# Kernel tuning notes

Hardware: AMD Instinct MI355X
Metric: run time of the kernel (lower is better)

Reference implementation:

```python
import jax, jax.numpy as jnp
import numpy as np

N = 50000      # nodes
E = 500000     # edges
D_IN = 512
D_H = 512
D_OUT = 256


def setup_inputs() -> dict:
    key = jax.random.key(0)
    ks = jax.random.split(key, 5)
    x = jax.random.normal(ks[0], (N, D_IN), dtype=jnp.float32)
    edge_index = jax.random.randint(ks[1], (2, E), 0, N, dtype=jnp.int32)
    W1 = jax.random.normal(ks[2], (D_IN, D_H), dtype=jnp.float32) / np.float32(np.sqrt(D_IN))
    b1 = jnp.zeros((D_H,), dtype=jnp.float32)
    W2 = jax.random.normal(ks[3], (D_H, D_OUT), dtype=jnp.float32) / np.float32(np.sqrt(D_H))
    b2 = jnp.zeros((D_OUT,), dtype=jnp.float32)
    return {"x": x, "edge_index": edge_index, "W1": W1, "b1": b1, "W2": W2, "b2": b2}


def _gcn_conv(x, src, dst, W, b, n):
    # PyG GCNConv: h = X W; add self-loops; symmetric norm D^-1/2 (A+I) D^-1/2; aggregate at dst; + bias
    h = x @ W
    loop = jnp.arange(n, dtype=src.dtype)
    src_sl = jnp.concatenate([src, loop])
    dst_sl = jnp.concatenate([dst, loop])
    deg = jax.ops.segment_sum(jnp.ones_like(src_sl, dtype=h.dtype), dst_sl, num_segments=n)
    dinv = jnp.where(deg > 0, jax.lax.rsqrt(deg), 0.0)
    norm = dinv[src_sl] * dinv[dst_sl]                     # [E+N]
    msg = h[src_sl] * norm[:, None]                        # [E+N, out]
    out = jax.ops.segment_sum(msg, dst_sl, num_segments=n) # [N, out]
    return out + b


def reference(x, edge_index, W1, b1, W2, b2):
    # Encoder.forward in eval mode (dropout = identity, bn='none' = identity), ELU activation after each conv.
    src, dst = edge_index[0], edge_index[1]
    h = _gcn_conv(x, src, dst, W1, b1, N)
    h = jax.nn.elu(h)
    h = _gcn_conv(h, src, dst, W2, b2, N)
    return jax.nn.elu(h)
```

## Files before the change

### kernel.cpp

```cpp
#include <hip/hip_runtime.h>
#include <math.h>

#define N_NODES 50000
#define N_EDGES 500000
#define D_IN 512
#define D_H  512
#define D_OUT 256
#define NB 196

typedef __attribute__((ext_vector_type(8))) short bf16x8;
typedef __attribute__((ext_vector_type(8))) unsigned short ushort8;
typedef __attribute__((ext_vector_type(4))) float f32x4;

__device__ __forceinline__ float b2f(unsigned short u) {
    union { unsigned int i; float f; } v; v.i = ((unsigned int)u) << 16; return v.f;
}
__device__ __forceinline__ unsigned short f2b(float f) {
    unsigned int x = __float_as_uint(f);
    unsigned int r = (x + 0x7fffu + ((x >> 16) & 1u)) >> 16;
    return (unsigned short)r;
}


__global__ __launch_bounds__(256) void k_cvt(const float* __restrict__ in,
                                             unsigned short* __restrict__ out,
                                             long long n8) {
    long long i = (long long)blockIdx.x * 256 + threadIdx.x;
    if (i >= n8) return;
    float4 v0 = ((const float4*)in)[i * 2];
    float4 v1 = ((const float4*)in)[i * 2 + 1];
    ushort8 o;
    o[0] = f2b(v0.x); o[1] = f2b(v0.y); o[2] = f2b(v0.z); o[3] = f2b(v0.w);
    o[4] = f2b(v1.x); o[5] = f2b(v1.y); o[6] = f2b(v1.z); o[7] = f2b(v1.w);
    ((ushort8*)out)[i] = o;
}


__global__ void k_wt(const float* __restrict__ W, unsigned short* __restrict__ Wt,
                     int K, int N) {
    __shared__ float t[32][33];
    const int bk = blockIdx.x * 32, bn = blockIdx.y * 32;
    const int tx = threadIdx.x, ty = threadIdx.y;
    for (int i = ty; i < 32; i += 8) t[i][tx] = W[(size_t)(bk + i) * N + bn + tx];
    __syncthreads();
    for (int i = ty; i < 32; i += 8)
        Wt[(size_t)(bn + i) * K + bk + tx] = f2b(t[tx][i]);
}


__global__ __launch_bounds__(256) void k_zero(int* __restrict__ p, int n) {
    int i = blockIdx.x * 256 + threadIdx.x;
    if (i < n) p[i] = 0;
}

__global__ __launch_bounds__(256) void k_indeg(const int* __restrict__ dst,
                                               int* __restrict__ indeg) {
    int i = blockIdx.x * 256 + threadIdx.x;
    if (i < N_EDGES) atomicAdd(&indeg[dst[i]], 1);
}

__global__ __launch_bounds__(256) void k_partials(const int* __restrict__ indeg,
                                                  int* __restrict__ bsum) {
    __shared__ int wsum[4];
    const int tid = threadIdx.x, lane = tid & 63, w = tid >> 6;
    const int i = blockIdx.x * 256 + tid;
    int v = (i < N_NODES) ? indeg[i] : 0;
#pragma unroll
    for (int o = 32; o > 0; o >>= 1) v += __shfl_down(v, o, 64);
    if (lane == 0) wsum[w] = v;
    __syncthreads();
    if (tid == 0) bsum[blockIdx.x] = wsum[0] + wsum[1] + wsum[2] + wsum[3];
}

__global__ __launch_bounds__(256) void k_scanb(const int* __restrict__ bsum,
                                               int* __restrict__ boff) {
    __shared__ int wsum[4];
    const int tid = threadIdx.x, lane = tid & 63, w = tid >> 6;
    const int v = (tid < NB) ? bsum[tid] : 0;
    int s = v;
#pragma unroll
    for (int o = 1; o < 64; o <<= 1) {
        int t = __shfl_up(s, o, 64);
        if (lane >= o) s += t;
    }
    if (lane == 63) wsum[w] = s;
    __syncthreads();
    int add = 0;
    for (int k = 0; k < w; ++k) add += wsum[k];
    if (tid < NB) boff[tid] = add + s - v;
}

__global__ __launch_bounds__(256) void k_finalize(const int* __restrict__ indeg,
                                                  const int* __restrict__ boff,
                                                  int* __restrict__ row_start,
                                                  int* __restrict__ cursor,
                                                  float* __restrict__ dinv) {
    __shared__ int wsum[4];
    const int tid = threadIdx.x, lane = tid & 63, w = tid >> 6;
    const int i = blockIdx.x * 256 + tid;
    const int v = (i < N_NODES) ? indeg[i] : 0;
    int s = v;
#pragma unroll
    for (int o = 1; o < 64; o <<= 1) {
        int t = __shfl_up(s, o, 64);
        if (lane >= o) s += t;
    }
    if (lane == 63) wsum[w] = s;
    __syncthreads();
    int add = boff[blockIdx.x];
    for (int k = 0; k < w; ++k) add += wsum[k];
    if (i < N_NODES) {
        const int excl = add + s - v;
        row_start[i] = excl;
        cursor[i] = excl;
        dinv[i] = rsqrtf((float)(1 + v));
    }
    if (i == N_NODES) row_start[N_NODES] = N_EDGES;
}

__global__ __launch_bounds__(256) void k_bucket(const int* __restrict__ src,
                                                const int* __restrict__ dst,
                                                int* __restrict__ cursor,
                                                int* __restrict__ csr_src) {
    int e = blockIdx.x * 256 + threadIdx.x;
    if (e >= N_EDGES) return;
    int pos = atomicAdd(&cursor[dst[e]], 1);
    csr_src[pos] = src[e];
}


__device__ __forceinline__ void gload16(const void* g, void* l) {
    __builtin_amdgcn_global_load_lds(
        (const __attribute__((address_space(1))) unsigned int*)g,
        (__attribute__((address_space(3))) unsigned int*)l, 16, 0, 0);
}

__global__ __launch_bounds__(256, 2) void k_gemm(const unsigned short* __restrict__ A,
                                                 const unsigned short* __restrict__ Bt,
                                                 unsigned short* __restrict__ C,
                                                 int M, int N, int K,
                                                 int ncb, int nrb) {
    __shared__ __align__(16) short As[2][128 * 64];
    __shared__ __align__(16) short Bs[2][128 * 64];

    const int bid = blockIdx.x;
    const int xcd = bid & 7;
    const int sidx = bid >> 3;
    const int cb = sidx % ncb;
    const int rb = (sidx / ncb) * 8 + xcd;
    if (rb >= nrb) return;
    const int brow = rb * 128;
    const int bcol = cb * 128;

    const int tid = threadIdx.x;
    const int wid = tid >> 6;
    const int lane = tid & 63;
    const int wr = wid >> 1, wc = wid & 1;
    const int lhi = lane >> 4, llo = lane & 15;

    f32x4 acc[4][4];
#pragma unroll
    for (int i = 0; i < 4; ++i)
#pragma unroll
        for (int j = 0; j < 4; ++j) acc[i][j] = (f32x4){0.f, 0.f, 0.f, 0.f};

#define STAGE(buf, kt)                                                          \
    {                                                                           \
        _Pragma("unroll") for (int g = 0; g < 4; ++g) {                         \
            const int s = g * 256 + tid;                                        \
            const int row = s >> 3;                                             \
            const int sc = (s & 7) ^ (row & 7);                                 \
            int gr = brow + row; gr = gr < M ? gr : M - 1;                      \
            gload16(A + (size_t)gr * K + (kt) + sc * 8,                         \
                    &As[buf][(g * 256 + wid * 64) * 8]);                        \
            gload16(Bt + (size_t)(bcol + row) * K + (kt) + sc * 8,              \
                    &Bs[buf][(g * 256 + wid * 64) * 8]);                        \
        }                                                                       \
    }

    const int nt = K / 64;

    STAGE(0, 0);
    __syncthreads();

    int cur = 0;
    for (int t = 0; t < nt; ++t) {
        if (t + 1 < nt) STAGE(cur ^ 1, (t + 1) * 64);

#pragma unroll
        for (int ks = 0; ks < 2; ++ks) {
            bf16x8 af[4], bf[4];
#pragma unroll
            for (int mi = 0; mi < 4; ++mi) {
                const int row = wr * 64 + mi * 16 + llo;
                af[mi] = *(const bf16x8*)&As[cur][row * 64 + (((ks * 4 + lhi) ^ (llo & 7)) * 8)];
            }
#pragma unroll
            for (int ni = 0; ni < 4; ++ni) {
                const int row = wc * 64 + ni * 16 + llo;
                bf[ni] = *(const bf16x8*)&Bs[cur][row * 64 + (((ks * 4 + lhi) ^ (llo & 7)) * 8)];
            }
#pragma unroll
            for (int mi = 0; mi < 4; ++mi)
#pragma unroll
                for (int ni = 0; ni < 4; ++ni)
                    acc[mi][ni] = __builtin_amdgcn_mfma_f32_16x16x32_bf16(
                        af[mi], bf[ni], acc[mi][ni], 0, 0, 0);
        }

        __syncthreads();
        cur ^= 1;
    }
#undef STAGE

    short* cws = &As[0][0] + wid * 4096;

#pragma unroll
    for (int mi = 0; mi < 4; ++mi)
#pragma unroll
        for (int ni = 0; ni < 4; ++ni) {
            const f32x4 v = acc[mi][ni];
#pragma unroll
            for (int r = 0; r < 4; ++r) {
                const int row = mi * 16 + lhi * 4 + r;
                const int col = ni * 16 + llo;
                const int chunk = (col >> 3) ^ (row & 7);
                cws[row * 64 + chunk * 8 + (col & 7)] = (short)f2b(v[r]);
            }
        }
    __syncthreads();

    {
        const int rsub = lane >> 3;
        const int c = lane & 7;
#pragma unroll
        for (int i = 0; i < 8; ++i) {
            const int row = i * 8 + rsub;
            const ushort8 o = *(const ushort8*)&cws[row * 64 + ((c ^ (row & 7)) * 8)];
            const int grow = brow + wr * 64 + row;
            if (grow < M)
                *(ushort8*)(C + (size_t)grow * N + bcol + wc * 64 + c * 8) = o;
        }
    }
}


template <int D, bool BF16_OUT>
__global__ __launch_bounds__(256) void k_aggregate(const unsigned short* __restrict__ H,
                                                   const float* __restrict__ bias,
                                                   void* __restrict__ outv,
                                                   const int* __restrict__ row_start,
                                                   const int* __restrict__ csr_src,
                                                   const float* __restrict__ dinv) {
    const int wid = threadIdx.x >> 6;
    const int lane = threadIdx.x & 63;
    int n, c0;
    if (D == 512) { n = blockIdx.x * 4 + wid; c0 = lane * 8; }
    else          { n = blockIdx.x * 8 + wid * 2 + (lane >> 5); c0 = (lane & 31) * 8; }
    if (n >= N_NODES) return;

    const float di = dinv[n];
    float acc[8];
    {
        const float ws = di * di;
        ushort8 v = *(const ushort8*)(H + (size_t)n * D + c0);
#pragma unroll
        for (int e = 0; e < 8; ++e) acc[e] = b2f(v[e]) * ws;
    }

    const int e0 = row_start[n];
    const int e1 = row_start[n + 1];
    int j = e0;
    for (; j + 8 <= e1; j += 8) {
        int s[8];
        float wgt[8];
#pragma unroll
        for (int q = 0; q < 8; ++q) s[q] = csr_src[j + q];
#pragma unroll
        for (int q = 0; q < 8; ++q) wgt[q] = dinv[s[q]] * di;
#pragma unroll
        for (int h = 0; h < 2; ++h) {
            const ushort8 v0 = *(const ushort8*)(H + (size_t)s[h * 4 + 0] * D + c0);
            const ushort8 v1 = *(const ushort8*)(H + (size_t)s[h * 4 + 1] * D + c0);
            const ushort8 v2 = *(const ushort8*)(H + (size_t)s[h * 4 + 2] * D + c0);
            const ushort8 v3 = *(const ushort8*)(H + (size_t)s[h * 4 + 3] * D + c0);
#pragma unroll
            for (int e = 0; e < 8; ++e) {
                acc[e] = fmaf(b2f(v0[e]), wgt[h * 4 + 0], acc[e]);
                acc[e] = fmaf(b2f(v1[e]), wgt[h * 4 + 1], acc[e]);
                acc[e] = fmaf(b2f(v2[e]), wgt[h * 4 + 2], acc[e]);
                acc[e] = fmaf(b2f(v3[e]), wgt[h * 4 + 3], acc[e]);
            }
        }
    }
    for (; j + 4 <= e1; j += 4) {
        const int s0 = csr_src[j + 0];
        const int s1 = csr_src[j + 1];
        const int s2 = csr_src[j + 2];
        const int s3 = csr_src[j + 3];
        const float w0 = dinv[s0] * di;
        const float w1 = dinv[s1] * di;
        const float w2 = dinv[s2] * di;
        const float w3 = dinv[s3] * di;
        const ushort8 v0 = *(const ushort8*)(H + (size_t)s0 * D + c0);
        const ushort8 v1 = *(const ushort8*)(H + (size_t)s1 * D + c0);
        const ushort8 v2 = *(const ushort8*)(H + (size_t)s2 * D + c0);
        const ushort8 v3 = *(const ushort8*)(H + (size_t)s3 * D + c0);
#pragma unroll
        for (int e = 0; e < 8; ++e) {
            acc[e] = fmaf(b2f(v0[e]), w0, acc[e]);
            acc[e] = fmaf(b2f(v1[e]), w1, acc[e]);
            acc[e] = fmaf(b2f(v2[e]), w2, acc[e]);
            acc[e] = fmaf(b2f(v3[e]), w3, acc[e]);
        }
    }
    for (; j < e1; ++j) {
        const int s = csr_src[j];
        const float ws = dinv[s] * di;
        const ushort8 v = *(const ushort8*)(H + (size_t)s * D + c0);
#pragma unroll
        for (int e = 0; e < 8; ++e) acc[e] = fmaf(b2f(v[e]), ws, acc[e]);
    }

#pragma unroll
    for (int e = 0; e < 8; ++e) {
        float t = acc[e] + bias[c0 + e];
        acc[e] = t > 0.f ? t : expf(t) - 1.f;
    }

    if (BF16_OUT) {
        ushort8 o;
#pragma unroll
        for (int e = 0; e < 8; ++e) o[e] = f2b(acc[e]);
        *(ushort8*)((unsigned short*)outv + (size_t)n * D + c0) = o;
    } else {
        float* orow = (float*)outv + (size_t)n * D + c0;
        *(float4*)orow = make_float4(acc[0], acc[1], acc[2], acc[3]);
        *(float4*)(orow + 4) = make_float4(acc[4], acc[5], acc[6], acc[7]);
    }
}


extern "C" void kernel_launch(void* const* d_in, const int* in_sizes, int n_in,
                              void* d_out, int out_size, void* d_ws, size_t ws_size,
                              hipStream_t stream) {
    const float* x  = (const float*)d_in[0];
    const int* ei   = (const int*)d_in[1];
    const int* src  = ei;
    const int* dst  = ei + N_EDGES;
    const float* W1 = (const float*)d_in[2];
    const float* b1 = (const float*)d_in[3];
    const float* W2 = (const float*)d_in[4];
    const float* b2 = (const float*)d_in[5];
    float* out = (float*)d_out;

    char* ws = (char*)d_ws;
    size_t off = 0;
    auto alloc = [&](size_t bytes) -> void* {
        void* p = ws + off;
        off = (off + bytes + 255) & ~(size_t)255;
        return p;
    };
    int*   indeg     = (int*)alloc((size_t)N_NODES * 4);
    int*   bsum      = (int*)alloc((size_t)NB * 4);
    int*   boff      = (int*)alloc((size_t)NB * 4);
    int*   row_start = (int*)alloc((size_t)(N_NODES + 1) * 4);
    int*   cursor    = (int*)alloc((size_t)N_NODES * 4);
    int*   csr_src   = (int*)alloc((size_t)N_EDGES * 4);
    float* dinv      = (float*)alloc((size_t)N_NODES * 4);
    unsigned short* W1t  = (unsigned short*)alloc((size_t)D_H * D_IN * 2);
    unsigned short* W2t  = (unsigned short*)alloc((size_t)D_OUT * D_H * 2);
    unsigned short* xb   = (unsigned short*)alloc((size_t)N_NODES * D_IN * 2);
    unsigned short* H1   = (unsigned short*)alloc((size_t)N_NODES * D_H * 2);
    unsigned short* out1 = (unsigned short*)alloc((size_t)N_NODES * D_H * 2);
    unsigned short* H2   = (unsigned short*)alloc((size_t)N_NODES * D_OUT * 2);

    k_zero<<<(N_NODES + 255) / 256, 256, 0, stream>>>(indeg, N_NODES);
    k_indeg<<<(N_EDGES + 255) / 256, 256, 0, stream>>>(dst, indeg);
    k_partials<<<NB, 256, 0, stream>>>(indeg, bsum);
    k_scanb<<<1, 256, 0, stream>>>(bsum, boff);
    k_finalize<<<NB, 256, 0, stream>>>(indeg, boff, row_start, cursor, dinv);
    k_bucket<<<(N_EDGES + 255) / 256, 256, 0, stream>>>(src, dst, cursor, csr_src);

    {
        const long long n8 = (long long)N_NODES * D_IN / 8;
        k_cvt<<<(int)((n8 + 255) / 256), 256, 0, stream>>>(x, xb, n8);
        dim3 b(32, 8);
        dim3 g1(D_IN / 32, D_H / 32);
        k_wt<<<g1, b, 0, stream>>>(W1, W1t, D_IN, D_H);
        dim3 g2(D_H / 32, D_OUT / 32);
        k_wt<<<g2, b, 0, stream>>>(W2, W2t, D_H, D_OUT);
    }

    const int nrb = (N_NODES + 127) / 128;
    const int rgrp = (nrb + 7) / 8;

    {
        const int ncb = D_H / 128;
        k_gemm<<<8 * ncb * rgrp, 256, 0, stream>>>(xb, W1t, H1, N_NODES, D_H, D_IN, ncb, nrb);
    }
    k_aggregate<512, true><<<(N_NODES + 3) / 4, 256, 0, stream>>>(H1, b1, out1, row_start, csr_src, dinv);

    {
        const int ncb = D_OUT / 128;
        k_gemm<<<8 * ncb * rgrp, 256, 0, stream>>>(out1, W2t, H2, N_NODES, D_OUT, D_H, ncb, nrb);
    }
    k_aggregate<256, false><<<(N_NODES + 7) / 8, 256, 0, stream>>>(H2, b2, out, row_start, csr_src, dinv);
}
```

Baseline: 294.8 us.

## Split aggregation into XCD-pinned column chunks for per-XCD L2 reuse

The aggregation kernel is rewritten so that each block covers a 32-column slice for 32 nodes. Block IDs are mapped so that blockIdx mod 8 picks the column chunk, which places each column slice on one XCD and lets its L2 cache hold only that slice of H during the gather. Each lane now loads 8-byte ushort4 values instead of 16-byte vectors, and the 8-edge unrolled loop is dropped. The cost is that csr_src, row_start and dinv are read more times (once per chunk), and the smaller loads plus less unrolling give less memory-level parallelism per thread.

```diff
diff --git a/kernel.cpp b/kernel.cpp
--- a/kernel.cpp
+++ b/kernel.cpp
@@ -245,54 +245,42 @@
 }
 
 
-template <int D, bool BF16_OUT>
-__global__ __launch_bounds__(256) void k_aggregate(const unsigned short* __restrict__ H,
+template <int D, bool BF16_OUT, int NPASS>
+__global__ __launch_bounds__(256) void k_agg_chunk(const unsigned short* __restrict__ H,
                                                    const float* __restrict__ bias,
                                                    void* __restrict__ outv,
                                                    const int* __restrict__ row_start,
                                                    const int* __restrict__ csr_src,
-                                                   const float* __restrict__ dinv) {
-    const int wid = threadIdx.x >> 6;
-    const int lane = threadIdx.x & 63;
-    int n, c0;
-    if (D == 512) { n = blockIdx.x * 4 + wid; c0 = lane * 8; }
-    else          { n = blockIdx.x * 8 + wid * 2 + (lane >> 5); c0 = (lane & 31) * 8; }
+                                                   const float* __restrict__ dinv,
+                                                   int nbpc) {
+    const int bid = blockIdx.x;
+    const int xcd = bid & 7;
+    const int s = bid >> 3;
+    const int pass = s / nbpc;
+    const int nb = s % nbpc;
+    const int col0 = (pass * 8 + xcd) * 32;
+
+    const int tid = threadIdx.x;
+    const int wid = tid >> 6;
+    const int lane = tid & 63;
+    const int grp = lane >> 3;
+    const int lg = lane & 7;
+
+    const int n = nb * 32 + wid * 8 + grp;
     if (n >= N_NODES) return;
+    const int c = col0 + lg * 4;
 
     const float di = dinv[n];
-    float acc[8];
-    {
-        const float ws = di * di;
-        ushort8 v = *(const ushort8*)(H + (size_t)n * D + c0);
-#pragma unroll
-        for (int e = 0; e < 8; ++e) acc[e] = b2f(v[e]) * ws;
+    float a0, a1, a2, a3;
+    {
+        const float w = di * di;
+        ushort4 v = *(const ushort4*)(H + (size_t)n * D + c);
+        a0 = b2f(v.x) * w; a1 = b2f(v.y) * w; a2 = b2f(v.z) * w; a3 = b2f(v.w) * w;
     }
 
     const int e0 = row_start[n];
     const int e1 = row_start[n + 1];
     int j = e0;
-    for (; j + 8 <= e1; j += 8) {
-        int s[8];
-        float wgt[8];
-#pragma unroll
-        for (int q = 0; q < 8; ++q) s[q] = csr_src[j + q];
-#pragma unroll
-        for (int q = 0; q < 8; ++q) wgt[q] = dinv[s[q]] * di;
-#pragma unroll
-        for (int h = 0; h < 2; ++h) {
-            const ushort8 v0 = *(const ushort8*)(H + (size_t)s[h * 4 + 0] * D + c0);
-            const ushort8 v1 = *(const ushort8*)(H + (size_t)s[h * 4 + 1] * D + c0);
-            const ushort8 v2 = *(const ushort8*)(H + (size_t)s[h * 4 + 2] * D + c0);
-            const ushort8 v3 = *(const ushort8*)(H + (size_t)s[h * 4 + 3] * D + c0);
-#pragma unroll
-            for (int e = 0; e < 8; ++e) {
-                acc[e] = fmaf(b2f(v0[e]), wgt[h * 4 + 0], acc[e]);
-                acc[e] = fmaf(b2f(v1[e]), wgt[h * 4 + 1], acc[e]);
-                acc[e] = fmaf(b2f(v2[e]), wgt[h * 4 + 2], acc[e]);
-                acc[e] = fmaf(b2f(v3[e]), wgt[h * 4 + 3], acc[e]);
-            }
-        }
-    }
     for (; j + 4 <= e1; j += 4) {
         const int s0 = csr_src[j + 0];
         const int s1 = csr_src[j + 1];
@@ -302,41 +290,40 @@
         const float w1 = dinv[s1] * di;
         const float w2 = dinv[s2] * di;
         const float w3 = dinv[s3] * di;
-        const ushort8 v0 = *(const ushort8*)(H + (size_t)s0 * D + c0);
-        const ushort8 v1 = *(const ushort8*)(H + (size_t)s1 * D + c0);
-        const ushort8 v2 = *(const ushort8*)(H + (size_t)s2 * D + c0);
-        const ushort8 v3 = *(const ushort8*)(H + (size_t)s3 * D + c0);
-#pragma unroll
-        for (int e = 0; e < 8; ++e) {
-            acc[e] = fmaf(b2f(v0[e]), w0, acc[e]);
-            acc[e] = fmaf(b2f(v1[e]), w1, acc[e]);
-            acc[e] = fmaf(b2f(v2[e]), w2, acc[e]);
-            acc[e] = fmaf(b2f(v3[e]), w3, acc[e]);
-        }
+        const ushort4 v0 = *(const ushort4*)(H + (size_t)s0 * D + c);
+        const ushort4 v1 = *(const ushort4*)(H + (size_t)s1 * D + c);
+        const ushort4 v2 = *(const ushort4*)(H + (size_t)s2 * D + c);
+        const ushort4 v3 = *(const ushort4*)(H + (size_t)s3 * D + c);
+        a0 = fmaf(b2f(v0.x), w0, a0); a1 = fmaf(b2f(v0.y), w0, a1);
+        a2 = fmaf(b2f(v0.z), w0, a2); a3 = fmaf(b2f(v0.w), w0, a3);
+        a0 = fmaf(b2f(v1.x), w1, a0); a1 = fmaf(b2f(v1.y), w1, a1);
+        a2 = fmaf(b2f(v1.z), w1, a2); a3 = fmaf(b2f(v1.w), w1, a3);
+        a0 = fmaf(b2f(v2.x), w2, a0); a1 = fmaf(b2f(v2.y), w2, a1);
+        a2 = fmaf(b2f(v2.z), w2, a2); a3 = fmaf(b2f(v2.w), w2, a3);
+        a0 = fmaf(b2f(v3.x), w3, a0); a1 = fmaf(b2f(v3.y), w3, a1);
+        a2 = fmaf(b2f(v3.z), w3, a2); a3 = fmaf(b2f(v3.w), w3, a3);
     }
     for (; j < e1; ++j) {
-        const int s = csr_src[j];
-        const float ws = dinv[s] * di;
-        const ushort8 v = *(const ushort8*)(H + (size_t)s * D + c0);
-#pragma unroll
-        for (int e = 0; e < 8; ++e) acc[e] = fmaf(b2f(v[e]), ws, acc[e]);
-    }
-
-#pragma unroll
-    for (int e = 0; e < 8; ++e) {
-        float t = acc[e] + bias[c0 + e];
-        acc[e] = t > 0.f ? t : expf(t) - 1.f;
-    }
+        const int sx = csr_src[j];
+        const float w = dinv[sx] * di;
+        const ushort4 v = *(const ushort4*)(H + (size_t)sx * D + c);
+        a0 = fmaf(b2f(v.x), w, a0); a1 = fmaf(b2f(v.y), w, a1);
+        a2 = fmaf(b2f(v.z), w, a2); a3 = fmaf(b2f(v.w), w, a3);
+    }
+
+    const float4 b = *(const float4*)(bias + c);
+    a0 += b.x; a1 += b.y; a2 += b.z; a3 += b.w;
+    a0 = a0 > 0.f ? a0 : expf(a0) - 1.f;
+    a1 = a1 > 0.f ? a1 : expf(a1) - 1.f;
+    a2 = a2 > 0.f ? a2 : expf(a2) - 1.f;
+    a3 = a3 > 0.f ? a3 : expf(a3) - 1.f;
 
     if (BF16_OUT) {
-        ushort8 o;
-#pragma unroll
-        for (int e = 0; e < 8; ++e) o[e] = f2b(acc[e]);
-        *(ushort8*)((unsigned short*)outv + (size_t)n * D + c0) = o;
+        ushort4 o;
+        o.x = f2b(a0); o.y = f2b(a1); o.z = f2b(a2); o.w = f2b(a3);
+        *(ushort4*)((unsigned short*)outv + (size_t)n * D + c) = o;
     } else {
-        float* orow = (float*)outv + (size_t)n * D + c0;
-        *(float4*)orow = make_float4(acc[0], acc[1], acc[2], acc[3]);
-        *(float4*)(orow + 4) = make_float4(acc[4], acc[5], acc[6], acc[7]);
+        *(float4*)((float*)outv + (size_t)n * D + c) = make_float4(a0, a1, a2, a3);
     }
 }
 
@@ -394,16 +381,19 @@
 
     const int nrb = (N_NODES + 127) / 128;
     const int rgrp = (nrb + 7) / 8;
+    const int nbpc = (N_NODES + 31) / 32;
 
     {
         const int ncb = D_H / 128;
         k_gemm<<<8 * ncb * rgrp, 256, 0, stream>>>(xb, W1t, H1, N_NODES, D_H, D_IN, ncb, nrb);
     }
-    k_aggregate<512, true><<<(N_NODES + 3) / 4, 256, 0, stream>>>(H1, b1, out1, row_start, csr_src, dinv);
+    k_agg_chunk<512, true, 2><<<8 * 2 * nbpc, 256, 0, stream>>>(
+        H1, b1, out1, row_start, csr_src, dinv, nbpc);
 
     {
         const int ncb = D_OUT / 128;
         k_gemm<<<8 * ncb * rgrp, 256, 0, stream>>>(out1, W2t, H2, N_NODES, D_OUT, D_H, ncb, nrb);
     }
-    k_aggregate<256, false><<<(N_NODES + 7) / 8, 256, 0, stream>>>(H2, b2, out, row_start, csr_src, dinv);
-}
+    k_agg_chunk<256, false, 1><<<8 * 1 * nbpc, 256, 0, stream>>>(
+        H2, b2, out, row_start, csr_src, dinv, nbpc);
+}
```

New measurement: 364.1 us. 1.24x slower.
